# Optimization experiments

Measured on AMD Instinct MI355X. Metric: run time of the kernel, lower is better.

## Reference

```python
import jax, jax.numpy as jnp
import numpy as np


def _gather_nbrs(feats, idx):
    # feats: [C, N], idx: [N, k] -> [C, N, k]
    return feats[:, idx]


def pointconv_dw(xyz, feats, idx, w_pos, b_pos, w_out, b_out):
    """Depthwise point conv: per-channel weights from relative neighbor coords.
    xyz: [B,3,N], feats: [B,C,N], idx: [B,N,k] -> [B,C_out,N]
    """
    nbr_xyz = jax.vmap(_gather_nbrs)(xyz, idx)            # [B,3,N,k]
    rel = nbr_xyz - xyz[:, :, :, None]                    # relative positions
    w = jnp.einsum('cd,bdnk->bcnk', w_pos, rel) + b_pos[None, :, None, None]
    g = jax.vmap(_gather_nbrs)(feats, idx)                # [B,C,N,k]
    agg = jnp.sum(w * g, axis=-1)                         # [B,C,N] depthwise reduce over k
    return jnp.einsum('oc,bcn->bon', w_out, agg) + b_out[None, :, None]


def setup_inputs() -> dict:
    key = jax.random.key(0)
    ks = jax.random.split(key, 16)
    B, N, K = 2, 65536, 4
    IN, HID = 64, 64
    C = HID + IN
    s = 0.02
    inp = {
        'xyz': jax.random.normal(ks[0], (B, 3, N), jnp.float32),
        'h': jax.random.normal(ks[1], (B, HID, N), jnp.float32),
        'x': jax.random.normal(ks[2], (B, IN, N), jnp.float32),
        'knn_indices': jax.random.randint(ks[3], (B, N, K), 0, N, jnp.int32),
    }
    names = ['z', 'r', 'q']
    for i, nm in enumerate(names):
        inp[f'w{nm}_pos'] = s * jax.random.normal(ks[4 + 4 * i], (C, 3), jnp.float32)
        inp[f'b{nm}_pos'] = jnp.zeros((C,), jnp.float32)
        inp[f'w{nm}_out'] = s * jax.random.normal(ks[5 + 4 * i], (HID, C), jnp.float32)
        inp[f'b{nm}_out'] = jnp.zeros((HID,), jnp.float32)
    return inp


def reference(xyz, h, x, knn_indices,
              wz_pos, bz_pos, wz_out, bz_out,
              wr_pos, br_pos, wr_out, br_out,
              wq_pos, bq_pos, wq_out, bq_out):
    hx = jnp.concatenate([h, x], axis=1)                  # [B, HID+IN, N]
    z = jax.nn.sigmoid(pointconv_dw(xyz, hx, knn_indices, wz_pos, bz_pos, wz_out, bz_out))
    r = jax.nn.sigmoid(pointconv_dw(xyz, hx, knn_indices, wr_pos, br_pos, wr_out, br_out))
    rhx = jnp.concatenate([r * h, x], axis=1)
    q = jnp.tanh(pointconv_dw(xyz, rhx, knn_indices, wq_pos, bq_pos, wq_out, bq_out))
    return (1.0 - z) * h + z * q
```

## Files before the change

### kernel.cpp

```cpp
#include <hip/hip_runtime.h>

#define NPTS 65536
#define BATCH 2
#define CCH 128
#define HIDC 64
#define LDB 520
#define LDB2 264
#define PLD 130

typedef unsigned short u16;
typedef unsigned int u32;
typedef __bf16 bf16_t;
typedef bf16_t bf16x8 __attribute__((ext_vector_type(8)));
typedef float f32x4 __attribute__((ext_vector_type(4)));
typedef float f32x2 __attribute__((ext_vector_type(2)));

__device__ __forceinline__ u16 f2bf(float f){
  union { float f; unsigned u; } v; v.f = f;
  unsigned r = v.u + 0x7FFFu + ((v.u >> 16) & 1u);
  return (u16)(r >> 16);
}
__device__ __forceinline__ float bf2f(u16 u){
  union { unsigned u; float f; } v; v.u = ((unsigned)u) << 16; return v.f;
}
__device__ __forceinline__ u32 pkrn(float a, float b){
  union { float f; u32 u; } ua, ub; ua.f = a; ub.f = b;
  return ((ua.u + 0x8000u) >> 16) | ((ub.u + 0x8000u) & 0xffff0000u);
}
__device__ __forceinline__ float sigmoidf_(float v){ return 1.f/(1.f+__expf(-v)); }
__device__ __forceinline__ float tanhf_(float v){
  v = fminf(10.f, fmaxf(-10.f, v));
  float e = __expf(2.f*v);
  return (e-1.f)/(e+1.f);
}

__global__ __launch_bounds__(256) void kprep(
    const float* __restrict__ wz, const float* __restrict__ wzp, const float* __restrict__ bzp,
    const float* __restrict__ wr, const float* __restrict__ wrp, const float* __restrict__ brp,
    const float* __restrict__ wq, const float* __restrict__ wqp, const float* __restrict__ bqp,
    u16* __restrict__ A){
  int idx = blockIdx.x*256 + threadIdx.x;
  if (idx < 98304){
    int t = idx & 7, o = (idx>>3)&63, quad = (idx>>9)&3, s = (idx>>11)&15, g = idx>>15;
    int pk = s*32 + quad*8 + t;
    int j = pk>>7, chunk = (pk>>3)&15, tt = pk&7;
    int orig = chunk*32 + j*8 + tt;
    int c = orig>>2, m = orig&3;
    const float* W  = (g==0)? wz  : (g==1)? wr  : wq;
    const float* wp = (g==0)? wzp : (g==1)? wrp : wqp;
    const float* bp = (g==0)? bzp : (g==1)? brp : bqp;
    float coef = m ? wp[c*3 + m - 1] : bp[c];
    A[idx] = f2bf(W[o*CCH + c] * coef);
  } else {
    int i2 = idx - 98304;
    int t = i2 & 7, o = (i2>>3)&63, quad = (i2>>9)&3, s = (i2>>11)&7;
    int k2 = s*32 + quad*8 + t;
    int j = k2>>6, chunk = (k2>>3)&7, tt = k2&7;
    int orig = chunk*32 + j*8 + tt;
    int c = orig>>2, m = orig&3;
    float coef = m ? wqp[c*3 + m - 1] : bqp[c];
    A[idx] = f2bf(wq[o*CCH + c] * coef);
  }
}

__global__ __launch_bounds__(256) void k_pack(const float* __restrict__ h,
    const float* __restrict__ x, u16* __restrict__ hxT){
  __shared__ __align__(16) u16 tile[64*PLD];
  int tid = threadIdx.x;
  int b = blockIdx.x >> 10, n0 = (blockIdx.x & 1023) << 6;
  #pragma unroll
  for (int i = 0; i < 8; ++i){
    int cc = (tid>>4) + i*16;
    int nn = (tid & 15)*4;
    const float* src = (cc < HIDC)
        ? (h + (((size_t)(b*HIDC + cc))<<16) + n0 + nn)
        : (x + (((size_t)(b*HIDC + cc - HIDC))<<16) + n0 + nn);
    float4 v = *(const float4*)src;
    tile[(nn+0)*PLD + cc] = f2bf(v.x);
    tile[(nn+1)*PLD + cc] = f2bf(v.y);
    tile[(nn+2)*PLD + cc] = f2bf(v.z);
    tile[(nn+3)*PLD + cc] = f2bf(v.w);
  }
  __syncthreads();
  #pragma unroll
  for (int i = 0; i < 4; ++i){
    int tsk = tid + (i<<8);
    int n = tsk>>4, ch = (tsk&15)*8;
    uint4 v = *(const uint4*)(tile + n*PLD + ch);
    *(uint4*)(hxT + (((size_t)(b<<16) + n0 + n)<<7) + ch) = v;
  }
}

#define ACCUM(gv, rv) { \
  u32 dw_[4] = {gv.x, gv.y, gv.z, gv.w}; \
  _Pragma("unroll") \
  for (int q_ = 0; q_ < 4; ++q_){ \
    union { u32 u; float f; } lo_, hi_; \
    lo_.u = dw_[q_] << 16; hi_.u = dw_[q_] & 0xffff0000u; \
    f32x2 v_ = {lo_.f, hi_.f}; \
    m0[q_] += v_; mx[q_] += rv.x * v_; my[q_] += rv.y * v_; mz[q_] += rv.z * v_; \
  } }

#define PACKROW(row, CHOFF, STRIDE) { \
  _Pragma("unroll") \
  for (int j_ = 0; j_ < 4; ++j_){ \
    uint4 v_; \
    v_.x = pkrn(m0[j_].x, mx[j_].x); v_.y = pkrn(my[j_].x, mz[j_].x); \
    v_.z = pkrn(m0[j_].y, mx[j_].y); v_.w = pkrn(my[j_].y, mz[j_].y); \
    *(uint4*)((row) + j_*(STRIDE) + (CHOFF)) = v_; \
  } }

#define MFMA_BF16(A_, B_, C_) __builtin_amdgcn_mfma_f32_16x16x32_bf16(A_, B_, C_, 0, 0, 0)

__global__ __launch_bounds__(256, 4) void k_zr(
    const float* __restrict__ xyz, const float* __restrict__ h,
    const int* __restrict__ knn,
    const float* __restrict__ bz_out, const float* __restrict__ br_out,
    const u16* __restrict__ Azr,
    const u16* __restrict__ hxT, u16* __restrict__ rhT,
    u16* __restrict__ z_ws, u16* __restrict__ qx_ws)
{
  __shared__ __align__(16) u16 bext[32*LDB];
  __shared__ __align__(16) float4 relk[128];
  __shared__ __align__(16) int4 jlds[32];

  int tid = threadIdx.x; int lane = tid & 63; int wv = tid >> 6;
  int b = blockIdx.x >> 11, n0 = (blockIdx.x & 2047) << 5;
  size_t bN = (size_t)b * NPTS;

  if (tid < 128){
    int p = tid >> 2, k = tid & 3;
    int j = knn[((bN + n0 + p) << 2) + k];
    ((int*)jlds)[tid] = j;
    const float* xb = xyz + (size_t)b*3*NPTS;
    float cx = xb[n0+p], cy = xb[NPTS + n0+p], cz = xb[2*NPTS + n0+p];
    relk[tid] = make_float4(xb[j]-cx, xb[NPTS+j]-cy, xb[2*NPTS+j]-cz, 0.f);
  }
  __syncthreads();

  const u16* hxTb = hxT + (bN << 7);
  int pA = tid >> 4, chk = tid & 15;
  int pB = pA + 16;
  int4 jA = jlds[pA], jB = jlds[pB];
  const u16* cb = hxTb + chk*8;
  uint4 ga0 = *(const uint4*)(cb + (((size_t)jA.x)<<7));
  uint4 ga1 = *(const uint4*)(cb + (((size_t)jA.y)<<7));
  uint4 ga2 = *(const uint4*)(cb + (((size_t)jA.z)<<7));
  uint4 ga3 = *(const uint4*)(cb + (((size_t)jA.w)<<7));
  uint4 gb0 = *(const uint4*)(cb + (((size_t)jB.x)<<7));
  uint4 gb1 = *(const uint4*)(cb + (((size_t)jB.y)<<7));
  uint4 gb2 = *(const uint4*)(cb + (((size_t)jB.z)<<7));
  uint4 gb3 = *(const uint4*)(cb + (((size_t)jB.w)<<7));
  {
    float4 r0 = relk[pA*4+0], r1 = relk[pA*4+1], r2 = relk[pA*4+2], r3 = relk[pA*4+3];
    f32x2 m0[4] = {{0,0},{0,0},{0,0},{0,0}}, mx[4] = {{0,0},{0,0},{0,0},{0,0}};
    f32x2 my[4] = {{0,0},{0,0},{0,0},{0,0}}, mz[4] = {{0,0},{0,0},{0,0},{0,0}};
    ACCUM(ga0, r0); ACCUM(ga1, r1); ACCUM(ga2, r2); ACCUM(ga3, r3);
    PACKROW(bext + pA*LDB, chk*8, 128);
  }
  {
    float4 r0 = relk[pB*4+0], r1 = relk[pB*4+1], r2 = relk[pB*4+2], r3 = relk[pB*4+3];
    f32x2 m0[4] = {{0,0},{0,0},{0,0},{0,0}}, mx[4] = {{0,0},{0,0},{0,0},{0,0}};
    f32x2 my[4] = {{0,0},{0,0},{0,0},{0,0}}, mz[4] = {{0,0},{0,0},{0,0},{0,0}};
    ACCUM(gb0, r0); ACCUM(gb1, r1); ACCUM(gb2, r2); ACCUM(gb3, r3);
    PACKROW(bext + pB*LDB, chk*8, 128);
  }
  __syncthreads();

  int l15 = lane & 15, quad = lane >> 4;
  int orow = wv*16 + l15;
  const u16* Abase = Azr + ((size_t)(quad*64 + orow))*8;

  f32x4 accz[2], accr[2], accq[2];
  #pragma unroll
  for (int nt = 0; nt < 2; ++nt){
    accz[nt] = (f32x4){0,0,0,0}; accr[nt] = (f32x4){0,0,0,0}; accq[nt] = (f32x4){0,0,0,0};
  }

  bf16x8 az0[4], ar0[4], aq0[2], az1[4], ar1[4], aq1[2];
#define LOADA(AZ, AR, AQ, SS) { \
  _Pragma("unroll") \
  for (int j = 0; j < 4; ++j){ \
    AZ[j] = *(const bf16x8*)(Abase + ((SS)*4 + j)*2048); \
    AR[j] = *(const bf16x8*)(Abase + 32768 + ((SS)*4 + j)*2048); \
  } \
  AQ[0] = *(const bf16x8*)(Abase + 65536 + ((SS)*4 + 2)*2048); \
  AQ[1] = *(const bf16x8*)(Abase + 65536 + ((SS)*4 + 3)*2048); }

#define MFMAG(AZ, AR, AQ, SS) { \
  _Pragma("unroll") \
  for (int j = 0; j < 4; ++j){ \
    int s_ = (SS)*4 + j; \
    _Pragma("unroll") \
    for (int nt = 0; nt < 2; ++nt){ \
      bf16x8 bb = *(const bf16x8*)(bext + (nt*16 + l15)*LDB + s_*32 + quad*8); \
      accz[nt] = MFMA_BF16(AZ[j], bb, accz[nt]); \
      accr[nt] = MFMA_BF16(AR[j], bb, accr[nt]); \
      if (j >= 2) accq[nt] = MFMA_BF16(AQ[j-2], bb, accq[nt]); \
    } } }

  LOADA(az0, ar0, aq0, 0);
  LOADA(az1, ar1, aq1, 1);
  MFMAG(az0, ar0, aq0, 0);
  LOADA(az0, ar0, aq0, 2);
  MFMAG(az1, ar1, aq1, 1);
  LOADA(az1, ar1, aq1, 3);
  MFMAG(az0, ar0, aq0, 2);
  MFMAG(az1, ar1, aq1, 3);

  __syncthreads();

  u16* zst  = bext;
  u16* rhst = bext + 2560;
  u16* qxst = bext + 2560 + 2304;
  #pragma unroll
  for (int nt = 0; nt < 2; ++nt){
    #pragma unroll
    for (int reg = 0; reg < 4; ++reg){
      int o = wv*16 + quad*4 + reg;
      int p = nt*16 + l15;
      float zf = sigmoidf_(accz[nt][reg] + bz_out[o]);
      float rf = sigmoidf_(accr[nt][reg] + br_out[o]);
      float hv = h[(((size_t)(b*HIDC + o))<<16) + n0 + p];
      zst[o*40 + p] = f2bf(zf);
      rhst[p*72 + o] = f2bf(rf * hv);
      qxst[o*40 + p] = f2bf(accq[nt][reg]);
    }
  }
  __syncthreads();

  {
    int p = tid >> 3, ch = (tid & 7)*8;
    uint4 v = *(const uint4*)(rhst + p*72 + ch);
    *(uint4*)(rhT + ((bN + n0 + p)<<6) + ch) = v;
  }
  {
    int o = tid >> 2, pc = (tid & 3)*8;
    uint4 v = *(const uint4*)(zst + o*40 + pc);
    *(uint4*)(z_ws + (((size_t)(b*HIDC + o))<<16) + n0 + pc) = v;
  }
  {
    int o = tid >> 2, pc = (tid & 3)*8;
    uint4 v = *(const uint4*)(qxst + o*40 + pc);
    *(uint4*)(qx_ws + (((size_t)(b*HIDC + o))<<16) + n0 + pc) = v;
  }
}

__global__ __launch_bounds__(256, 4) void k_q(
    const float* __restrict__ xyz, const float* __restrict__ h,
    const int* __restrict__ knn,
    const float* __restrict__ bq_out,
    const u16* __restrict__ Aqrh,
    const u16* __restrict__ rhT, const u16* __restrict__ z_ws,
    const u16* __restrict__ qx_ws, float* __restrict__ out)
{
  __shared__ __align__(16) u16 bext[64*LDB2];
  __shared__ __align__(16) float4 relk[256];
  __shared__ __align__(16) int4 jlds[64];

  int tid = threadIdx.x; int lane = tid & 63; int wv = tid >> 6;
  int b = blockIdx.x >> 10, n0 = (blockIdx.x & 1023) << 6;
  size_t bN = (size_t)b * NPTS;

  {
    int p = tid >> 2, k = tid & 3;
    int j = knn[((bN + n0 + p) << 2) + k];
    ((int*)jlds)[tid] = j;
    const float* xb = xyz + (size_t)b*3*NPTS;
    float cx = xb[n0+p], cy = xb[NPTS + n0+p], cz = xb[2*NPTS + n0+p];
    relk[tid] = make_float4(xb[j]-cx, xb[NPTS+j]-cy, xb[2*NPTS+j]-cz, 0.f);
  }
  __syncthreads();

  const u16* rhTb = rhT + (bN << 6);
  int pA = tid >> 3, chk = tid & 7;
  int pB = pA + 32;
  int4 jA = jlds[pA], jB = jlds[pB];
  const u16* cb = rhTb + chk*8;
  uint4 ga0 = *(const uint4*)(cb + (((size_t)jA.x)<<6));
  uint4 ga1 = *(const uint4*)(cb + (((size_t)jA.y)<<6));
  uint4 ga2 = *(const uint4*)(cb + (((size_t)jA.z)<<6));
  uint4 ga3 = *(const uint4*)(cb + (((size_t)jA.w)<<6));
  uint4 gb0 = *(const uint4*)(cb + (((size_t)jB.x)<<6));
  uint4 gb1 = *(const uint4*)(cb + (((size_t)jB.y)<<6));
  uint4 gb2 = *(const uint4*)(cb + (((size_t)jB.z)<<6));
  uint4 gb3 = *(const uint4*)(cb + (((size_t)jB.w)<<6));
  {
    float4 r0 = relk[pA*4+0], r1 = relk[pA*4+1], r2 = relk[pA*4+2], r3 = relk[pA*4+3];
    f32x2 m0[4] = {{0,0},{0,0},{0,0},{0,0}}, mx[4] = {{0,0},{0,0},{0,0},{0,0}};
    f32x2 my[4] = {{0,0},{0,0},{0,0},{0,0}}, mz[4] = {{0,0},{0,0},{0,0},{0,0}};
    ACCUM(ga0, r0); ACCUM(ga1, r1); ACCUM(ga2, r2); ACCUM(ga3, r3);
    PACKROW(bext + pA*LDB2, chk*8, 64);
  }
  {
    float4 r0 = relk[pB*4+0], r1 = relk[pB*4+1], r2 = relk[pB*4+2], r3 = relk[pB*4+3];
    f32x2 m0[4] = {{0,0},{0,0},{0,0},{0,0}}, mx[4] = {{0,0},{0,0},{0,0},{0,0}};
    f32x2 my[4] = {{0,0},{0,0},{0,0},{0,0}}, mz[4] = {{0,0},{0,0},{0,0},{0,0}};
    ACCUM(gb0, r0); ACCUM(gb1, r1); ACCUM(gb2, r2); ACCUM(gb3, r3);
    PACKROW(bext + pB*LDB2, chk*8, 64);
  }
  __syncthreads();

  int l15 = lane & 15, quad = lane >> 4;
  int orow = wv*16 + l15;
  const u16* Abase = Aqrh + ((size_t)(quad*64 + orow))*8;
  f32x4 acc[4];
  #pragma unroll
  for (int nt = 0; nt < 4; ++nt) acc[nt] = (f32x4){0,0,0,0};

  bf16x8 a0[4], a1[4];
#define LOADAQ(AQ, SS) { \
  _Pragma("unroll") \
  for (int j = 0; j < 4; ++j) AQ[j] = *(const bf16x8*)(Abase + ((SS)*4 + j)*2048); }

#define MFMAGQ(AQ, SS) { \
  _Pragma("unroll") \
  for (int j = 0; j < 4; ++j){ \
    int s_ = (SS)*4 + j; \
    _Pragma("unroll") \
    for (int nt = 0; nt < 4; ++nt){ \
      bf16x8 bb = *(const bf16x8*)(bext + (nt*16 + l15)*LDB2 + s_*32 + quad*8); \
      acc[nt] = MFMA_BF16(AQ[j], bb, acc[nt]); \
    } } }

  LOADAQ(a0, 0);
  LOADAQ(a1, 1);
  MFMAGQ(a0, 0);
  MFMAGQ(a1, 1);

  #pragma unroll
  for (int nt = 0; nt < 4; ++nt){
    #pragma unroll
    for (int reg = 0; reg < 4; ++reg){
      int o = wv*16 + quad*4 + reg;
      int p = nt*16 + l15;
      size_t idx = (((size_t)(b*HIDC + o))<<16) + n0 + p;
      float qpre = acc[nt][reg] + bq_out[o] + bf2f(qx_ws[idx]);
      float qf = tanhf_(qpre);
      float zf = bf2f(z_ws[idx]);
      float hv = h[idx];
      out[idx] = (1.f - zf)*hv + zf*qf;
    }
  }
}

extern "C" void kernel_launch(void* const* d_in, const int* in_sizes, int n_in,
                              void* d_out, int out_size, void* d_ws, size_t ws_size,
                              hipStream_t stream){
  const float* xyz    = (const float*)d_in[0];
  const float* h      = (const float*)d_in[1];
  const float* x      = (const float*)d_in[2];
  const int*   knn    = (const int*)d_in[3];
  const float* wz_pos = (const float*)d_in[4];
  const float* bz_pos = (const float*)d_in[5];
  const float* wz_out = (const float*)d_in[6];
  const float* bz_out = (const float*)d_in[7];
  const float* wr_pos = (const float*)d_in[8];
  const float* br_pos = (const float*)d_in[9];
  const float* wr_out = (const float*)d_in[10];
  const float* br_out = (const float*)d_in[11];
  const float* wq_pos = (const float*)d_in[12];
  const float* bq_pos = (const float*)d_in[13];
  const float* wq_out = (const float*)d_in[14];
  const float* bq_out = (const float*)d_in[15];
  float* out = (float*)d_out;

  u16* ws    = (u16*)d_ws;
  u16* hxT   = ws;
  u16* rhT   = ws + 16777216;
  u16* z_ws  = ws + 25165824;
  u16* qx_ws = ws + 33554432;
  u16* A     = ws + 41943040;

  kprep<<<448, 256, 0, stream>>>(wz_out, wz_pos, bz_pos, wr_out, wr_pos, br_pos,
                                 wq_out, wq_pos, bq_pos, A);
  k_pack<<<2048, 256, 0, stream>>>(h, x, hxT);
  k_zr<<<4096, 256, 0, stream>>>(xyz, h, knn, bz_out, br_out, A, hxT, rhT, z_ws, qx_ws);
  k_q<<<2048, 256, 0, stream>>>(xyz, h, knn, bq_out, A + 98304, rhT, z_ws, qx_ws, out);
}
```

Before: 224.3 us.

## Process two point tiles per block with software-pipelined gathers and packed z/q workspace

Each block of k_zr and k_q now handles two 32-point tiles. The neighbor gather for the second tile is issued while the MFMAs of the first tile run, and h and the workspace values are prefetched into registers ahead of the epilogue. z and q-partial are interleaved into a single u32 workspace so k_q does one load instead of two. Lighter barriers that wait only on LDS traffic (lgkmcnt) replace __syncthreads. This is meant to hide gather latency, but it raises register pressure and depends on hand-placed sched barriers.

```diff
diff --git a/kernel.cpp b/kernel.cpp
--- a/kernel.cpp
+++ b/kernel.cpp
@@ -32,6 +32,12 @@
   v = fminf(10.f, fmaxf(-10.f, v));
   float e = __expf(2.f*v);
   return (e-1.f)/(e+1.f);
+}
+
+__device__ __forceinline__ void bar_lgkm(){
+  asm volatile("s_waitcnt lgkmcnt(0)" ::: "memory");
+  __builtin_amdgcn_s_barrier();
+  __builtin_amdgcn_sched_barrier(0);
 }
 
 __global__ __launch_bounds__(256) void kprep(
@@ -118,66 +124,66 @@
     const float* __restrict__ bz_out, const float* __restrict__ br_out,
     const u16* __restrict__ Azr,
     const u16* __restrict__ hxT, u16* __restrict__ rhT,
-    u16* __restrict__ z_ws, u16* __restrict__ qx_ws)
+    u32* __restrict__ zq_ws)
 {
   __shared__ __align__(16) u16 bext[32*LDB];
-  __shared__ __align__(16) float4 relk[128];
-  __shared__ __align__(16) int4 jlds[32];
+  __shared__ __align__(16) float4 relk[2][128];
+  __shared__ __align__(16) int4 jlds[2][32];
 
   int tid = threadIdx.x; int lane = tid & 63; int wv = tid >> 6;
-  int b = blockIdx.x >> 11, n0 = (blockIdx.x & 2047) << 5;
+  int l15 = lane & 15, quad = lane >> 4;
+  int b = blockIdx.x >> 10, nb = (blockIdx.x & 1023) << 6;
   size_t bN = (size_t)b * NPTS;
 
-  if (tid < 128){
-    int p = tid >> 2, k = tid & 3;
-    int j = knn[((bN + n0 + p) << 2) + k];
+  {
+    int t_ = tid >> 7, p_ = (tid >> 2) & 31, k_ = tid & 3;
+    int n_ = nb + t_*32 + p_;
+    int j = knn[((bN + n_) << 2) + k_];
     ((int*)jlds)[tid] = j;
     const float* xb = xyz + (size_t)b*3*NPTS;
-    float cx = xb[n0+p], cy = xb[NPTS + n0+p], cz = xb[2*NPTS + n0+p];
-    relk[tid] = make_float4(xb[j]-cx, xb[NPTS+j]-cy, xb[2*NPTS+j]-cz, 0.f);
-  }
-  __syncthreads();
+    float cx = xb[n_], cy = xb[NPTS + n_], cz = xb[2*NPTS + n_];
+    relk[t_][p_*4 + k_] = make_float4(xb[j]-cx, xb[NPTS+j]-cy, xb[2*NPTS+j]-cz, 0.f);
+  }
+  float hp0[8];
+  #pragma unroll
+  for (int nt = 0; nt < 2; ++nt)
+    #pragma unroll
+    for (int reg = 0; reg < 4; ++reg)
+      hp0[nt*4+reg] = h[(((size_t)(b*HIDC + wv*16 + quad*4 + reg))<<16) + nb + nt*16 + l15];
+  bar_lgkm();
 
   const u16* hxTb = hxT + (bN << 7);
   int pA = tid >> 4, chk = tid & 15;
-  int pB = pA + 16;
-  int4 jA = jlds[pA], jB = jlds[pB];
-  const u16* cb = hxTb + chk*8;
-  uint4 ga0 = *(const uint4*)(cb + (((size_t)jA.x)<<7));
-  uint4 ga1 = *(const uint4*)(cb + (((size_t)jA.y)<<7));
-  uint4 ga2 = *(const uint4*)(cb + (((size_t)jA.z)<<7));
-  uint4 ga3 = *(const uint4*)(cb + (((size_t)jA.w)<<7));
-  uint4 gb0 = *(const uint4*)(cb + (((size_t)jB.x)<<7));
-  uint4 gb1 = *(const uint4*)(cb + (((size_t)jB.y)<<7));
-  uint4 gb2 = *(const uint4*)(cb + (((size_t)jB.z)<<7));
-  uint4 gb3 = *(const uint4*)(cb + (((size_t)jB.w)<<7));
-  {
-    float4 r0 = relk[pA*4+0], r1 = relk[pA*4+1], r2 = relk[pA*4+2], r3 = relk[pA*4+3];
-    f32x2 m0[4] = {{0,0},{0,0},{0,0},{0,0}}, mx[4] = {{0,0},{0,0},{0,0},{0,0}};
-    f32x2 my[4] = {{0,0},{0,0},{0,0},{0,0}}, mz[4] = {{0,0},{0,0},{0,0},{0,0}};
-    ACCUM(ga0, r0); ACCUM(ga1, r1); ACCUM(ga2, r2); ACCUM(ga3, r3);
-    PACKROW(bext + pA*LDB, chk*8, 128);
-  }
-  {
-    float4 r0 = relk[pB*4+0], r1 = relk[pB*4+1], r2 = relk[pB*4+2], r3 = relk[pB*4+3];
-    f32x2 m0[4] = {{0,0},{0,0},{0,0},{0,0}}, mx[4] = {{0,0},{0,0},{0,0},{0,0}};
-    f32x2 my[4] = {{0,0},{0,0},{0,0},{0,0}}, mz[4] = {{0,0},{0,0},{0,0},{0,0}};
-    ACCUM(gb0, r0); ACCUM(gb1, r1); ACCUM(gb2, r2); ACCUM(gb3, r3);
-    PACKROW(bext + pB*LDB, chk*8, 128);
-  }
-  __syncthreads();
-
-  int l15 = lane & 15, quad = lane >> 4;
+  const u16* cbp = hxTb + chk*8;
+
+#define GATH_ZR(G, JL) { \
+  int4 jA_ = (JL)[pA], jB_ = (JL)[pA+16]; \
+  G[0] = *(const uint4*)(cbp + (((size_t)jA_.x)<<7)); \
+  G[1] = *(const uint4*)(cbp + (((size_t)jA_.y)<<7)); \
+  G[2] = *(const uint4*)(cbp + (((size_t)jA_.z)<<7)); \
+  G[3] = *(const uint4*)(cbp + (((size_t)jA_.w)<<7)); \
+  G[4] = *(const uint4*)(cbp + (((size_t)jB_.x)<<7)); \
+  G[5] = *(const uint4*)(cbp + (((size_t)jB_.y)<<7)); \
+  G[6] = *(const uint4*)(cbp + (((size_t)jB_.z)<<7)); \
+  G[7] = *(const uint4*)(cbp + (((size_t)jB_.w)<<7)); }
+
+#define MOMPACK_ZR(G, RK) { \
+  { float4 r0 = (RK)[pA*4+0], r1 = (RK)[pA*4+1], r2 = (RK)[pA*4+2], r3 = (RK)[pA*4+3]; \
+    f32x2 m0[4] = {{0,0},{0,0},{0,0},{0,0}}, mx[4] = {{0,0},{0,0},{0,0},{0,0}}; \
+    f32x2 my[4] = {{0,0},{0,0},{0,0},{0,0}}, mz[4] = {{0,0},{0,0},{0,0},{0,0}}; \
+    ACCUM(G[0], r0); ACCUM(G[1], r1); ACCUM(G[2], r2); ACCUM(G[3], r3); \
+    PACKROW(bext + pA*LDB, chk*8, 128); } \
+  { float4 r0 = (RK)[(pA+16)*4+0], r1 = (RK)[(pA+16)*4+1], r2 = (RK)[(pA+16)*4+2], r3 = (RK)[(pA+16)*4+3]; \
+    f32x2 m0[4] = {{0,0},{0,0},{0,0},{0,0}}, mx[4] = {{0,0},{0,0},{0,0},{0,0}}; \
+    f32x2 my[4] = {{0,0},{0,0},{0,0},{0,0}}, mz[4] = {{0,0},{0,0},{0,0},{0,0}}; \
+    ACCUM(G[4], r0); ACCUM(G[5], r1); ACCUM(G[6], r2); ACCUM(G[7], r3); \
+    PACKROW(bext + (pA+16)*LDB, chk*8, 128); } }
+
   int orow = wv*16 + l15;
   const u16* Abase = Azr + ((size_t)(quad*64 + orow))*8;
-
   f32x4 accz[2], accr[2], accq[2];
-  #pragma unroll
-  for (int nt = 0; nt < 2; ++nt){
-    accz[nt] = (f32x4){0,0,0,0}; accr[nt] = (f32x4){0,0,0,0}; accq[nt] = (f32x4){0,0,0,0};
-  }
-
   bf16x8 az0[4], ar0[4], aq0[2], az1[4], ar1[4], aq1[2];
+
 #define LOADA(AZ, AR, AQ, SS) { \
   _Pragma("unroll") \
   for (int j = 0; j < 4; ++j){ \
@@ -199,6 +205,69 @@
       if (j >= 2) accq[nt] = MFMA_BF16(AQ[j-2], bb, accq[nt]); \
     } } }
 
+#define EPI_ZR(HP, N0) { \
+  u32* zqst = (u32*)bext;             \
+  u16* rhst = bext + 5120;            \
+  _Pragma("unroll") \
+  for (int nt = 0; nt < 2; ++nt){ \
+    _Pragma("unroll") \
+    for (int reg = 0; reg < 4; ++reg){ \
+      int o = wv*16 + quad*4 + reg; \
+      int p = nt*16 + l15; \
+      float zf = sigmoidf_(accz[nt][reg] + bz_out[o]); \
+      float rf = sigmoidf_(accr[nt][reg] + br_out[o]); \
+      zqst[o*40 + p] = (u32)f2bf(zf) | (((u32)f2bf(accq[nt][reg])) << 16); \
+      rhst[p*72 + o] = f2bf(rf * HP[nt*4+reg]); \
+    } } \
+  bar_lgkm(); \
+  _Pragma("unroll") \
+  for (int i_ = 0; i_ < 2; ++i_){ \
+    int task = tid + (i_<<8); \
+    int o = task >> 3, c4 = (task & 7)*4; \
+    uint4 v = *(const uint4*)(zqst + o*40 + c4); \
+    *(uint4*)(zq_ws + (((size_t)(b*HIDC + o))<<16) + (N0) + c4) = v; \
+  } \
+  { int p = tid >> 3, ch = (tid & 7)*8; \
+    uint4 v = *(const uint4*)(rhst + p*72 + ch); \
+    *(uint4*)(rhT + ((bN + (N0) + p)<<6) + ch) = v; } }
+
+  uint4 g0[8], g1[8];
+  GATH_ZR(g0, jlds[0]);
+  __builtin_amdgcn_sched_barrier(0);
+  MOMPACK_ZR(g0, relk[0]);
+  bar_lgkm();
+
+  #pragma unroll
+  for (int nt = 0; nt < 2; ++nt){
+    accz[nt] = (f32x4){0,0,0,0}; accr[nt] = (f32x4){0,0,0,0}; accq[nt] = (f32x4){0,0,0,0};
+  }
+  LOADA(az0, ar0, aq0, 0);
+  LOADA(az1, ar1, aq1, 1);
+  MFMAG(az0, ar0, aq0, 0);
+  LOADA(az0, ar0, aq0, 2);
+  MFMAG(az1, ar1, aq1, 1);
+  LOADA(az1, ar1, aq1, 3);
+  GATH_ZR(g1, jlds[1]);
+  __builtin_amdgcn_sched_barrier(0);
+  MFMAG(az0, ar0, aq0, 2);
+  MFMAG(az1, ar1, aq1, 3);
+  bar_lgkm();
+
+  EPI_ZR(hp0, nb);
+  float hp1[8];
+  #pragma unroll
+  for (int nt = 0; nt < 2; ++nt)
+    #pragma unroll
+    for (int reg = 0; reg < 4; ++reg)
+      hp1[nt*4+reg] = h[(((size_t)(b*HIDC + wv*16 + quad*4 + reg))<<16) + nb + 32 + nt*16 + l15];
+  bar_lgkm();
+
+  MOMPACK_ZR(g1, relk[1]);
+  bar_lgkm();
+  #pragma unroll
+  for (int nt = 0; nt < 2; ++nt){
+    accz[nt] = (f32x4){0,0,0,0}; accr[nt] = (f32x4){0,0,0,0}; accq[nt] = (f32x4){0,0,0,0};
+  }
   LOADA(az0, ar0, aq0, 0);
   LOADA(az1, ar1, aq1, 1);
   MFMAG(az0, ar0, aq0, 0);
@@ -207,43 +276,8 @@
   LOADA(az1, ar1, aq1, 3);
   MFMAG(az0, ar0, aq0, 2);
   MFMAG(az1, ar1, aq1, 3);
-
-  __syncthreads();
-
-  u16* zst  = bext;
-  u16* rhst = bext + 2560;
-  u16* qxst = bext + 2560 + 2304;
-  #pragma unroll
-  for (int nt = 0; nt < 2; ++nt){
-    #pragma unroll
-    for (int reg = 0; reg < 4; ++reg){
-      int o = wv*16 + quad*4 + reg;
-      int p = nt*16 + l15;
-      float zf = sigmoidf_(accz[nt][reg] + bz_out[o]);
-      float rf = sigmoidf_(accr[nt][reg] + br_out[o]);
-      float hv = h[(((size_t)(b*HIDC + o))<<16) + n0 + p];
-      zst[o*40 + p] = f2bf(zf);
-      rhst[p*72 + o] = f2bf(rf * hv);
-      qxst[o*40 + p] = f2bf(accq[nt][reg]);
-    }
-  }
-  __syncthreads();
-
-  {
-    int p = tid >> 3, ch = (tid & 7)*8;
-    uint4 v = *(const uint4*)(rhst + p*72 + ch);
-    *(uint4*)(rhT + ((bN + n0 + p)<<6) + ch) = v;
-  }
-  {
-    int o = tid >> 2, pc = (tid & 3)*8;
-    uint4 v = *(const uint4*)(zst + o*40 + pc);
-    *(uint4*)(z_ws + (((size_t)(b*HIDC + o))<<16) + n0 + pc) = v;
-  }
-  {
-    int o = tid >> 2, pc = (tid & 3)*8;
-    uint4 v = *(const uint4*)(qxst + o*40 + pc);
-    *(uint4*)(qx_ws + (((size_t)(b*HIDC + o))<<16) + n0 + pc) = v;
-  }
+  bar_lgkm();
+  EPI_ZR(hp1, nb + 32);
 }
 
 __global__ __launch_bounds__(256, 4) void k_q(
@@ -251,64 +285,61 @@
     const int* __restrict__ knn,
     const float* __restrict__ bq_out,
     const u16* __restrict__ Aqrh,
-    const u16* __restrict__ rhT, const u16* __restrict__ z_ws,
-    const u16* __restrict__ qx_ws, float* __restrict__ out)
+    const u16* __restrict__ rhT, const u32* __restrict__ zq_ws,
+    float* __restrict__ out)
 {
-  __shared__ __align__(16) u16 bext[64*LDB2];
-  __shared__ __align__(16) float4 relk[256];
-  __shared__ __align__(16) int4 jlds[64];
+  __shared__ __align__(16) u16 bext[32*LDB2];
+  __shared__ __align__(16) float4 relk[2][128];
+  __shared__ __align__(16) int4 jlds[2][32];
 
   int tid = threadIdx.x; int lane = tid & 63; int wv = tid >> 6;
-  int b = blockIdx.x >> 10, n0 = (blockIdx.x & 1023) << 6;
+  int l15 = lane & 15, quad = lane >> 4;
+  int b = blockIdx.x >> 10, nb = (blockIdx.x & 1023) << 6;
   size_t bN = (size_t)b * NPTS;
 
   {
-    int p = tid >> 2, k = tid & 3;
-    int j = knn[((bN + n0 + p) << 2) + k];
+    int t_ = tid >> 7, p_ = (tid >> 2) & 31, k_ = tid & 3;
+    int n_ = nb + t_*32 + p_;
+    int j = knn[((bN + n_) << 2) + k_];
     ((int*)jlds)[tid] = j;
     const float* xb = xyz + (size_t)b*3*NPTS;
-    float cx = xb[n0+p], cy = xb[NPTS + n0+p], cz = xb[2*NPTS + n0+p];
-    relk[tid] = make_float4(xb[j]-cx, xb[NPTS+j]-cy, xb[2*NPTS+j]-cz, 0.f);
-  }
-  __syncthreads();
+    float cx = xb[n_], cy = xb[NPTS + n_], cz = xb[2*NPTS + n_];
+    relk[t_][p_*4 + k_] = make_float4(xb[j]-cx, xb[NPTS+j]-cy, xb[2*NPTS+j]-cz, 0.f);
+  }
+  float hs0[8]; u32 zq0[8];
+  #pragma unroll
+  for (int nt = 0; nt < 2; ++nt)
+    #pragma unroll
+    for (int reg = 0; reg < 4; ++reg){
+      size_t idx = (((size_t)(b*HIDC + wv*16 + quad*4 + reg))<<16) + nb + nt*16 + l15;
+      hs0[nt*4+reg] = h[idx];
+      zq0[nt*4+reg] = zq_ws[idx];
+    }
+  bar_lgkm();
 
   const u16* rhTb = rhT + (bN << 6);
   int pA = tid >> 3, chk = tid & 7;
-  int pB = pA + 32;
-  int4 jA = jlds[pA], jB = jlds[pB];
-  const u16* cb = rhTb + chk*8;
-  uint4 ga0 = *(const uint4*)(cb + (((size_t)jA.x)<<6));
-  uint4 ga1 = *(const uint4*)(cb + (((size_t)jA.y)<<6));
-  uint4 ga2 = *(const uint4*)(cb + (((size_t)jA.z)<<6));
-  uint4 ga3 = *(const uint4*)(cb + (((size_t)jA.w)<<6));
-  uint4 gb0 = *(const uint4*)(cb + (((size_t)jB.x)<<6));
-  uint4 gb1 = *(const uint4*)(cb + (((size_t)jB.y)<<6));
-  uint4 gb2 = *(const uint4*)(cb + (((size_t)jB.z)<<6));
-  uint4 gb3 = *(const uint4*)(cb + (((size_t)jB.w)<<6));
-  {
-    float4 r0 = relk[pA*4+0], r1 = relk[pA*4+1], r2 = relk[pA*4+2], r3 = relk[pA*4+3];
-    f32x2 m0[4] = {{0,0},{0,0},{0,0},{0,0}}, mx[4] = {{0,0},{0,0},{0,0},{0,0}};
-    f32x2 my[4] = {{0,0},{0,0},{0,0},{0,0}}, mz[4] = {{0,0},{0,0},{0,0},{0,0}};
-    ACCUM(ga0, r0); ACCUM(ga1, r1); ACCUM(ga2, r2); ACCUM(ga3, r3);
-    PACKROW(bext + pA*LDB2, chk*8, 64);
-  }
-  {
-    float4 r0 = relk[pB*4+0], r1 = relk[pB*4+1], r2 = relk[pB*4+2], r3 = relk[pB*4+3];
-    f32x2 m0[4] = {{0,0},{0,0},{0,0},{0,0}}, mx[4] = {{0,0},{0,0},{0,0},{0,0}};
-    f32x2 my[4] = {{0,0},{0,0},{0,0},{0,0}}, mz[4] = {{0,0},{0,0},{0,0},{0,0}};
-    ACCUM(gb0, r0); ACCUM(gb1, r1); ACCUM(gb2, r2); ACCUM(gb3, r3);
-    PACKROW(bext + pB*LDB2, chk*8, 64);
-  }
-  __syncthreads();
-
-  int l15 = lane & 15, quad = lane >> 4;
+  const u16* cbq = rhTb + chk*8;
+
+#define GATH_Q(G, JL) { \
+  int4 jA_ = (JL)[pA]; \
+  G[0] = *(const uint4*)(cbq + (((size_t)jA_.x)<<6)); \
+  G[1] = *(const uint4*)(cbq + (((size_t)jA_.y)<<6)); \
+  G[2] = *(const uint4*)(cbq + (((size_t)jA_.z)<<6)); \
+  G[3] = *(const uint4*)(cbq + (((size_t)jA_.w)<<6)); }
+
+#define MOMPACK_Q(G, RK) { \
+  float4 r0 = (RK)[pA*4+0], r1 = (RK)[pA*4+1], r2 = (RK)[pA*4+2], r3 = (RK)[pA*4+3]; \
+  f32x2 m0[4] = {{0,0},{0,0},{0,0},{0,0}}, mx[4] = {{0,0},{0,0},{0,0},{0,0}}; \
+  f32x2 my[4] = {{0,0},{0,0},{0,0},{0,0}}, mz[4] = {{0,0},{0,0},{0,0},{0,0}}; \
+  ACCUM(G[0], r0); ACCUM(G[1], r1); ACCUM(G[2], r2); ACCUM(G[3], r3); \
+  PACKROW(bext + pA*LDB2, chk*8, 64); }
+
   int orow = wv*16 + l15;
   const u16* Abase = Aqrh + ((size_t)(quad*64 + orow))*8;
-  f32x4 acc[4];
-  #pragma unroll
-  for (int nt = 0; nt < 4; ++nt) acc[nt] = (f32x4){0,0,0,0};
-
+  f32x4 acc[2];
   bf16x8 a0[4], a1[4];
+
 #define LOADAQ(AQ, SS) { \
   _Pragma("unroll") \
   for (int j = 0; j < 4; ++j) AQ[j] = *(const bf16x8*)(Abase + ((SS)*4 + j)*2048); }
@@ -318,30 +349,60 @@
   for (int j = 0; j < 4; ++j){ \
     int s_ = (SS)*4 + j; \
     _Pragma("unroll") \
-    for (int nt = 0; nt < 4; ++nt){ \
+    for (int nt = 0; nt < 2; ++nt){ \
       bf16x8 bb = *(const bf16x8*)(bext + (nt*16 + l15)*LDB2 + s_*32 + quad*8); \
       acc[nt] = MFMA_BF16(AQ[j], bb, acc[nt]); \
     } } }
 
+#define EPI_Q(HS, ZQ, N0) { \
+  _Pragma("unroll") \
+  for (int nt = 0; nt < 2; ++nt){ \
+    _Pragma("unroll") \
+    for (int reg = 0; reg < 4; ++reg){ \
+      int o = wv*16 + quad*4 + reg; \
+      int p = nt*16 + l15; \
+      size_t idx = (((size_t)(b*HIDC + o))<<16) + (N0) + p; \
+      u32 zqv = ZQ[nt*4+reg]; \
+      float qpre = acc[nt][reg] + bq_out[o] + bf2f((u16)(zqv >> 16)); \
+      float qf = tanhf_(qpre); \
+      float zf = bf2f((u16)(zqv & 0xffffu)); \
+      out[idx] = (1.f - zf)*HS[nt*4+reg] + zf*qf; \
+    } } }
+
+  uint4 g0[4], g1[4];
+  GATH_Q(g0, jlds[0]);
+  __builtin_amdgcn_sched_barrier(0);
+  MOMPACK_Q(g0, relk[0]);
+  bar_lgkm();
+
+  acc[0] = (f32x4){0,0,0,0}; acc[1] = (f32x4){0,0,0,0};
+  LOADAQ(a0, 0);
+  LOADAQ(a1, 1);
+  MFMAGQ(a0, 0);
+  GATH_Q(g1, jlds[1]);
+  __builtin_amdgcn_sched_barrier(0);
+  MFMAGQ(a1, 1);
+  bar_lgkm();
+
+  EPI_Q(hs0, zq0, nb);
+  float hs1[8]; u32 zq1[8];
+  #pragma unroll
+  for (int nt = 0; nt < 2; ++nt)
+    #pragma unroll
+    for (int reg = 0; reg < 4; ++reg){
+      size_t idx = (((size_t)(b*HIDC + wv*16 + quad*4 + reg))<<16) + nb + 32 + nt*16 + l15;
+      hs1[nt*4+reg] = h[idx];
+      zq1[nt*4+reg] = zq_ws[idx];
+    }
+
+  MOMPACK_Q(g1, relk[1]);
+  bar_lgkm();
+  acc[0] = (f32x4){0,0,0,0}; acc[1] = (f32x4){0,0,0,0};
   LOADAQ(a0, 0);
   LOADAQ(a1, 1);
   MFMAGQ(a0, 0);
   MFMAGQ(a1, 1);
-
-  #pragma unroll
-  for (int nt = 0; nt < 4; ++nt){
-    #pragma unroll
-    for (int reg = 0; reg < 4; ++reg){
-      int o = wv*16 + quad*4 + reg;
-      int p = nt*16 + l15;
-      size_t idx = (((size_t)(b*HIDC + o))<<16) + n0 + p;
-      float qpre = acc[nt][reg] + bq_out[o] + bf2f(qx_ws[idx]);
-      float qf = tanhf_(qpre);
-      float zf = bf2f(z_ws[idx]);
-      float hv = h[idx];
-      out[idx] = (1.f - zf)*hv + zf*qf;
-    }
-  }
+  EPI_Q(hs1, zq1, nb + 32);
 }
 
 extern "C" void kernel_launch(void* const* d_in, const int* in_sizes, int n_in,
@@ -368,13 +429,12 @@
   u16* ws    = (u16*)d_ws;
   u16* hxT   = ws;
   u16* rhT   = ws + 16777216;
-  u16* z_ws  = ws + 25165824;
-  u16* qx_ws = ws + 33554432;
+  u32* zq_ws = (u32*)(ws + 25165824);
   u16* A     = ws + 41943040;
 
   kprep<<<448, 256, 0, stream>>>(wz_out, wz_pos, bz_pos, wr_out, wr_pos, br_pos,
                                  wq_out, wq_pos, bq_pos, A);
   k_pack<<<2048, 256, 0, stream>>>(h, x, hxT);
-  k_zr<<<4096, 256, 0, stream>>>(xyz, h, knn, bz_out, br_out, A, hxT, rhT, z_ws, qx_ws);
-  k_q<<<2048, 256, 0, stream>>>(xyz, h, knn, bq_out, A + 98304, rhT, z_ws, qx_ws, out);
-}
+  k_zr<<<2048, 256, 0, stream>>>(xyz, h, knn, bz_out, br_out, A, hxT, rhT, zq_ws);
+  k_q<<<2048, 256, 0, stream>>>(xyz, h, knn, bq_out, A + 98304, rhT, zq_ws, out);
+}
```

New measurement: 280.8 us. 25.2% more time.

## Merge prep/pack kernels, interleave z and q workspace, read h from bf16 cache

Applied to the files above, without the earlier changes.

Fuses the weight-prep and h/x pack kernels into one launch, removing a kernel boundary. k_zr now reads h from the already-packed bf16 hxT buffer instead of the fp32 h array, and writes z and q-preactivation interleaved into one u32 workspace, so k_q does a single load per element and prefetches h and zq before the gather phase. This cuts launch overhead and global traffic, at the cost of extra registers in k_q and bf16-rounded h in the r*h product.

```diff
diff --git a/kernel.cpp b/kernel.cpp
--- a/kernel.cpp
+++ b/kernel.cpp
@@ -34,60 +34,60 @@
   return (e-1.f)/(e+1.f);
 }
 
-__global__ __launch_bounds__(256) void kprep(
+__global__ __launch_bounds__(256) void k_prep_pack(
+    const float* __restrict__ h, const float* __restrict__ x, u16* __restrict__ hxT,
     const float* __restrict__ wz, const float* __restrict__ wzp, const float* __restrict__ bzp,
     const float* __restrict__ wr, const float* __restrict__ wrp, const float* __restrict__ brp,
     const float* __restrict__ wq, const float* __restrict__ wqp, const float* __restrict__ bqp,
     u16* __restrict__ A){
-  int idx = blockIdx.x*256 + threadIdx.x;
-  if (idx < 98304){
-    int t = idx & 7, o = (idx>>3)&63, quad = (idx>>9)&3, s = (idx>>11)&15, g = idx>>15;
-    int pk = s*32 + quad*8 + t;
-    int j = pk>>7, chunk = (pk>>3)&15, tt = pk&7;
-    int orig = chunk*32 + j*8 + tt;
-    int c = orig>>2, m = orig&3;
-    const float* W  = (g==0)? wz  : (g==1)? wr  : wq;
-    const float* wp = (g==0)? wzp : (g==1)? wrp : wqp;
-    const float* bp = (g==0)? bzp : (g==1)? brp : bqp;
-    float coef = m ? wp[c*3 + m - 1] : bp[c];
-    A[idx] = f2bf(W[o*CCH + c] * coef);
-  } else {
-    int i2 = idx - 98304;
-    int t = i2 & 7, o = (i2>>3)&63, quad = (i2>>9)&3, s = (i2>>11)&7;
-    int k2 = s*32 + quad*8 + t;
-    int j = k2>>6, chunk = (k2>>3)&7, tt = k2&7;
-    int orig = chunk*32 + j*8 + tt;
-    int c = orig>>2, m = orig&3;
-    float coef = m ? wqp[c*3 + m - 1] : bqp[c];
-    A[idx] = f2bf(wq[o*CCH + c] * coef);
-  }
-}
-
-__global__ __launch_bounds__(256) void k_pack(const float* __restrict__ h,
-    const float* __restrict__ x, u16* __restrict__ hxT){
   __shared__ __align__(16) u16 tile[64*PLD];
   int tid = threadIdx.x;
-  int b = blockIdx.x >> 10, n0 = (blockIdx.x & 1023) << 6;
-  #pragma unroll
-  for (int i = 0; i < 8; ++i){
-    int cc = (tid>>4) + i*16;
-    int nn = (tid & 15)*4;
-    const float* src = (cc < HIDC)
-        ? (h + (((size_t)(b*HIDC + cc))<<16) + n0 + nn)
-        : (x + (((size_t)(b*HIDC + cc - HIDC))<<16) + n0 + nn);
-    float4 v = *(const float4*)src;
-    tile[(nn+0)*PLD + cc] = f2bf(v.x);
-    tile[(nn+1)*PLD + cc] = f2bf(v.y);
-    tile[(nn+2)*PLD + cc] = f2bf(v.z);
-    tile[(nn+3)*PLD + cc] = f2bf(v.w);
-  }
-  __syncthreads();
-  #pragma unroll
-  for (int i = 0; i < 4; ++i){
-    int tsk = tid + (i<<8);
-    int n = tsk>>4, ch = (tsk&15)*8;
-    uint4 v = *(const uint4*)(tile + n*PLD + ch);
-    *(uint4*)(hxT + (((size_t)(b<<16) + n0 + n)<<7) + ch) = v;
+  if (blockIdx.x < 2048){
+    int b = blockIdx.x >> 10, n0 = (blockIdx.x & 1023) << 6;
+    #pragma unroll
+    for (int i = 0; i < 8; ++i){
+      int cc = (tid>>4) + i*16;
+      int nn = (tid & 15)*4;
+      const float* src = (cc < HIDC)
+          ? (h + (((size_t)(b*HIDC + cc))<<16) + n0 + nn)
+          : (x + (((size_t)(b*HIDC + cc - HIDC))<<16) + n0 + nn);
+      float4 v = *(const float4*)src;
+      tile[(nn+0)*PLD + cc] = f2bf(v.x);
+      tile[(nn+1)*PLD + cc] = f2bf(v.y);
+      tile[(nn+2)*PLD + cc] = f2bf(v.z);
+      tile[(nn+3)*PLD + cc] = f2bf(v.w);
+    }
+    __syncthreads();
+    #pragma unroll
+    for (int i = 0; i < 4; ++i){
+      int tsk = tid + (i<<8);
+      int n = tsk>>4, ch = (tsk&15)*8;
+      uint4 v = *(const uint4*)(tile + n*PLD + ch);
+      *(uint4*)(hxT + (((size_t)(b<<16) + n0 + n)<<7) + ch) = v;
+    }
+  } else {
+    int idx = (blockIdx.x - 2048)*256 + tid;
+    if (idx < 98304){
+      int t = idx & 7, o = (idx>>3)&63, quad = (idx>>9)&3, s = (idx>>11)&15, g = idx>>15;
+      int pk = s*32 + quad*8 + t;
+      int j = pk>>7, chunk = (pk>>3)&15, tt = pk&7;
+      int orig = chunk*32 + j*8 + tt;
+      int c = orig>>2, m = orig&3;
+      const float* W  = (g==0)? wz  : (g==1)? wr  : wq;
+      const float* wp = (g==0)? wzp : (g==1)? wrp : wqp;
+      const float* bp = (g==0)? bzp : (g==1)? brp : bqp;
+      float coef = m ? wp[c*3 + m - 1] : bp[c];
+      A[idx] = f2bf(W[o*CCH + c] * coef);
+    } else {
+      int i2 = idx - 98304;
+      int t = i2 & 7, o = (i2>>3)&63, quad = (i2>>9)&3, s = (i2>>11)&7;
+      int k2 = s*32 + quad*8 + t;
+      int j = k2>>6, chunk = (k2>>3)&7, tt = k2&7;
+      int orig = chunk*32 + j*8 + tt;
+      int c = orig>>2, m = orig&3;
+      float coef = m ? wqp[c*3 + m - 1] : bqp[c];
+      A[idx] = f2bf(wq[o*CCH + c] * coef);
+    }
   }
 }
 
@@ -113,20 +113,26 @@
 #define MFMA_BF16(A_, B_, C_) __builtin_amdgcn_mfma_f32_16x16x32_bf16(A_, B_, C_, 0, 0, 0)
 
 __global__ __launch_bounds__(256, 4) void k_zr(
-    const float* __restrict__ xyz, const float* __restrict__ h,
+    const float* __restrict__ xyz,
     const int* __restrict__ knn,
     const float* __restrict__ bz_out, const float* __restrict__ br_out,
     const u16* __restrict__ Azr,
     const u16* __restrict__ hxT, u16* __restrict__ rhT,
-    u16* __restrict__ z_ws, u16* __restrict__ qx_ws)
+    u32* __restrict__ zq_ws)
 {
   __shared__ __align__(16) u16 bext[32*LDB];
   __shared__ __align__(16) float4 relk[128];
   __shared__ __align__(16) int4 jlds[32];
 
   int tid = threadIdx.x; int lane = tid & 63; int wv = tid >> 6;
+  int l15 = lane & 15, quad = lane >> 4;
   int b = blockIdx.x >> 11, n0 = (blockIdx.x & 2047) << 5;
   size_t bN = (size_t)b * NPTS;
+
+  uint2 hraw[2];
+  #pragma unroll
+  for (int nt = 0; nt < 2; ++nt)
+    hraw[nt] = *(const uint2*)(hxT + ((bN + n0 + nt*16 + l15)<<7) + wv*16 + quad*4);
 
   if (tid < 128){
     int p = tid >> 2, k = tid & 3;
@@ -167,7 +173,6 @@
   }
   __syncthreads();
 
-  int l15 = lane & 15, quad = lane >> 4;
   int orow = wv*16 + l15;
   const u16* Abase = Azr + ((size_t)(quad*64 + orow))*8;
 
@@ -210,22 +215,24 @@
 
   __syncthreads();
 
-  u16* zst  = bext;
-  u16* rhst = bext + 2560;
-  u16* qxst = bext + 2560 + 2304;
+  u32* zqst = (u32*)bext;
+  u16* rhst = bext + 5632;
   #pragma unroll
   for (int nt = 0; nt < 2; ++nt){
+    u32 hr = nt ? hraw[1].x : hraw[0].x;
     #pragma unroll
     for (int reg = 0; reg < 4; ++reg){
       int o = wv*16 + quad*4 + reg;
       int p = nt*16 + l15;
+      u32 hw = (reg < 2) ? hraw[nt].x : hraw[nt].y;
+      u16 hu = (reg & 1) ? (u16)(hw >> 16) : (u16)(hw & 0xffffu);
+      float hv = bf2f(hu);
       float zf = sigmoidf_(accz[nt][reg] + bz_out[o]);
       float rf = sigmoidf_(accr[nt][reg] + br_out[o]);
-      float hv = h[(((size_t)(b*HIDC + o))<<16) + n0 + p];
-      zst[o*40 + p] = f2bf(zf);
+      zqst[o*44 + p] = (u32)f2bf(zf) | (((u32)f2bf(accq[nt][reg])) << 16);
       rhst[p*72 + o] = f2bf(rf * hv);
-      qxst[o*40 + p] = f2bf(accq[nt][reg]);
-    }
+    }
+    (void)hr;
   }
   __syncthreads();
 
@@ -234,15 +241,12 @@
     uint4 v = *(const uint4*)(rhst + p*72 + ch);
     *(uint4*)(rhT + ((bN + n0 + p)<<6) + ch) = v;
   }
-  {
-    int o = tid >> 2, pc = (tid & 3)*8;
-    uint4 v = *(const uint4*)(zst + o*40 + pc);
-    *(uint4*)(z_ws + (((size_t)(b*HIDC + o))<<16) + n0 + pc) = v;
-  }
-  {
-    int o = tid >> 2, pc = (tid & 3)*8;
-    uint4 v = *(const uint4*)(qxst + o*40 + pc);
-    *(uint4*)(qx_ws + (((size_t)(b*HIDC + o))<<16) + n0 + pc) = v;
+  #pragma unroll
+  for (int i = 0; i < 2; ++i){
+    int task = tid + (i<<8);
+    int o = task >> 3, c4 = (task & 7)*4;
+    uint4 v = *(const uint4*)(zqst + o*44 + c4);
+    *(uint4*)(zq_ws + (((size_t)(b*HIDC + o))<<16) + n0 + c4) = v;
   }
 }
 
@@ -251,16 +255,27 @@
     const int* __restrict__ knn,
     const float* __restrict__ bq_out,
     const u16* __restrict__ Aqrh,
-    const u16* __restrict__ rhT, const u16* __restrict__ z_ws,
-    const u16* __restrict__ qx_ws, float* __restrict__ out)
+    const u16* __restrict__ rhT, const u32* __restrict__ zq_ws,
+    float* __restrict__ out)
 {
   __shared__ __align__(16) u16 bext[64*LDB2];
   __shared__ __align__(16) float4 relk[256];
   __shared__ __align__(16) int4 jlds[64];
 
   int tid = threadIdx.x; int lane = tid & 63; int wv = tid >> 6;
+  int l15 = lane & 15, quad = lane >> 4;
   int b = blockIdx.x >> 10, n0 = (blockIdx.x & 1023) << 6;
   size_t bN = (size_t)b * NPTS;
+
+  float hs[16]; u32 zqp[16];
+  #pragma unroll
+  for (int nt = 0; nt < 4; ++nt)
+    #pragma unroll
+    for (int reg = 0; reg < 4; ++reg){
+      size_t idx = (((size_t)(b*HIDC + wv*16 + quad*4 + reg))<<16) + n0 + nt*16 + l15;
+      hs[nt*4+reg] = h[idx];
+      zqp[nt*4+reg] = zq_ws[idx];
+    }
 
   {
     int p = tid >> 2, k = tid & 3;
@@ -301,7 +316,6 @@
   }
   __syncthreads();
 
-  int l15 = lane & 15, quad = lane >> 4;
   int orow = wv*16 + l15;
   const u16* Abase = Aqrh + ((size_t)(quad*64 + orow))*8;
   f32x4 acc[4];
@@ -335,11 +349,11 @@
       int o = wv*16 + quad*4 + reg;
       int p = nt*16 + l15;
       size_t idx = (((size_t)(b*HIDC + o))<<16) + n0 + p;
-      float qpre = acc[nt][reg] + bq_out[o] + bf2f(qx_ws[idx]);
+      u32 zqv = zqp[nt*4+reg];
+      float qpre = acc[nt][reg] + bq_out[o] + bf2f((u16)(zqv >> 16));
       float qf = tanhf_(qpre);
-      float zf = bf2f(z_ws[idx]);
-      float hv = h[idx];
-      out[idx] = (1.f - zf)*hv + zf*qf;
+      float zf = bf2f((u16)(zqv & 0xffffu));
+      out[idx] = (1.f - zf)*hs[nt*4+reg] + zf*qf;
     }
   }
 }
@@ -368,13 +382,11 @@
   u16* ws    = (u16*)d_ws;
   u16* hxT   = ws;
   u16* rhT   = ws + 16777216;
-  u16* z_ws  = ws + 25165824;
-  u16* qx_ws = ws + 33554432;
+  u32* zq_ws = (u32*)(ws + 25165824);
   u16* A     = ws + 41943040;
 
-  kprep<<<448, 256, 0, stream>>>(wz_out, wz_pos, bz_pos, wr_out, wr_pos, br_pos,
-                                 wq_out, wq_pos, bq_pos, A);
-  k_pack<<<2048, 256, 0, stream>>>(h, x, hxT);
-  k_zr<<<4096, 256, 0, stream>>>(xyz, h, knn, bz_out, br_out, A, hxT, rhT, z_ws, qx_ws);
-  k_q<<<2048, 256, 0, stream>>>(xyz, h, knn, bq_out, A + 98304, rhT, z_ws, qx_ws, out);
-}
+  k_prep_pack<<<2496, 256, 0, stream>>>(h, x, hxT,
+      wz_out, wz_pos, bz_pos, wr_out, wr_pos, br_pos, wq_out, wq_pos, bq_pos, A);
+  k_zr<<<4096, 256, 0, stream>>>(xyz, knn, bz_out, br_out, A, hxT, rhT, zq_ws);
+  k_q<<<2048, 256, 0, stream>>>(xyz, h, knn, bq_out, A + 98304, rhT, zq_ws, out);
+}
```

Result: no change. 222.2 us (-1.0%).
